# Kernel tuning notes

Hardware: AMD Instinct MI355X
Metric: run time of the kernel (lower is better)

The kernel has to match this reference:

```python
import jax, jax.numpy as jnp
import numpy as np

N, IN_F, OUT_F, R = 8192, 4096, 4096, 16
ALPHA = 32
SCALING = ALPHA / R  # 2.0


def setup_inputs() -> dict:
    key = jax.random.key(0)
    k1, k2, k3, k4, k5 = jax.random.split(key, 5)
    return {
        "x": jax.random.normal(k1, (N, IN_F), dtype=jnp.float32),
        "W": jax.random.normal(k2, (OUT_F, IN_F), dtype=jnp.float32) * 0.02,
        "b": jax.random.normal(k3, (OUT_F,), dtype=jnp.float32) * 0.02,
        "lora_A": jax.random.normal(k4, (R, IN_F), dtype=jnp.float32) * 0.02,
        "lora_B": jax.random.normal(k5, (OUT_F, R), dtype=jnp.float32) * 0.02,
    }


def reference(x, W, b, lora_A, lora_B):
    # Base linear: x [N, in_f] @ W.T [in_f, out_f] + b -> [N, out_f]
    result = jnp.einsum('ni,oi->no', x, W) + b
    # LoRA path: (B @ (A @ x.T)).T * scaling == (x @ A.T) @ B.T * scaling
    lora = jnp.einsum('nr,or->no', jnp.einsum('ni,ri->nr', x, lora_A), lora_B)
    return result + lora * SCALING
```

## Files before the change

### kernel.cpp

```cpp
#include <hip/hip_runtime.h>
#include <hip/hip_bf16.h>
#include <stdint.h>

#define N_ROWS 8192
#define IN_F   4096
#define OUT_F  4096
#define R_LORA 16
#define KP     4160

typedef __bf16 bf16_t;
typedef __attribute__((ext_vector_type(8))) __bf16 bf16x8;
typedef __attribute__((ext_vector_type(4))) __bf16 bf16x4;
typedef __attribute__((ext_vector_type(4))) float  f32x4;
typedef __attribute__((ext_vector_type(16))) float f32x16;

__device__ __forceinline__ void load16_lds(const bf16_t* g, bf16_t* l) {
    auto gp = (const __attribute__((address_space(1))) void*)g;
    auto lp = (__attribute__((address_space(3))) void*)(uint32_t)(uintptr_t)l;
    __builtin_amdgcn_global_load_lds(gp, lp, 16, 0, 0);
}

#define PREPA_BLOCKS 2048

__global__ __launch_bounds__(256) void prep_fused(const float* __restrict__ x,
                                                  const float* __restrict__ W,
                                                  const float* __restrict__ bias,
                                                  const float* __restrict__ lA,
                                                  const float* __restrict__ lB,
                                                  bf16_t* __restrict__ Aw,
                                                  bf16_t* __restrict__ Bw) {
    int b = blockIdx.x;
    int t = threadIdx.x;
    if (b < PREPA_BLOCKS) {
        int row0 = b * 4;
        for (int rr = 0; rr < 4; ++rr) {
            int row = row0 + rr;
            const float4* xr = (const float4*)(x + (size_t)row * IN_F);
            bf16_t* ar = Aw + (size_t)row * KP;
            for (int s = t; s < 512; s += 256) {
                float4 f0 = xr[2 * s];
                float4 f1 = xr[2 * s + 1];
                bf16x8 v;
                v[0] = (bf16_t)f0.x; v[1] = (bf16_t)f0.y;
                v[2] = (bf16_t)f0.z; v[3] = (bf16_t)f0.w;
                v[4] = (bf16_t)f1.x; v[5] = (bf16_t)f1.y;
                v[6] = (bf16_t)f1.z; v[7] = (bf16_t)f1.w;
                *(bf16x8*)(ar + s * 8) = v;
            }
            if (t < 64) ar[IN_F + t] = (t == 0) ? (bf16_t)1.0f : (bf16_t)0.0f;
        }
    } else {
        int o0 = (b - PREPA_BLOCKS) * 4;
        float bl[4][R_LORA];
        for (int oo = 0; oo < 4; ++oo)
            for (int r = 0; r < R_LORA; ++r)
                bl[oo][r] = 2.0f * lB[(o0 + oo) * R_LORA + r];

        for (int j = 0; j < IN_F / (256 * 4); ++j) {
            int i4 = (j * 256 + t) * 4;
            f32x4 acc[4];
            for (int oo = 0; oo < 4; ++oo) {
                float4 w = *(const float4*)(W + (size_t)(o0 + oo) * IN_F + i4);
                acc[oo] = (f32x4){w.x, w.y, w.z, w.w};
            }
            for (int r = 0; r < R_LORA; ++r) {
                float4 a = *(const float4*)(lA + (size_t)r * IN_F + i4);
                for (int oo = 0; oo < 4; ++oo) {
                    acc[oo][0] += bl[oo][r] * a.x;
                    acc[oo][1] += bl[oo][r] * a.y;
                    acc[oo][2] += bl[oo][r] * a.z;
                    acc[oo][3] += bl[oo][r] * a.w;
                }
            }
            for (int oo = 0; oo < 4; ++oo) {
                bf16x4 v;
                v[0] = (bf16_t)acc[oo][0]; v[1] = (bf16_t)acc[oo][1];
                v[2] = (bf16_t)acc[oo][2]; v[3] = (bf16_t)acc[oo][3];
                *(bf16x4*)(Bw + (size_t)(o0 + oo) * KP + i4) = v;
            }
        }
        {
            int oo = t >> 6;
            int c  = IN_F + (t & 63);
            float v = (c == IN_F) ? bias[o0 + oo] : 0.0f;
            Bw[(size_t)(o0 + oo) * KP + c] = (bf16_t)v;
        }
    }
}

#define BM 256
#define BN 256
#define BK 64
#define NT (KP / BK)

__global__ __launch_bounds__(512, 2) void gemm_bt(const bf16_t* __restrict__ A,
                                                  const bf16_t* __restrict__ B,
                                                  float* __restrict__ C) {
    __shared__ __align__(16) bf16_t lds[2][2][BM * BK];

    int bid = blockIdx.x;
    int swz = (bid & 7) * 64 + (bid >> 3);
    int bm  = swz & 31;
    int bn  = swz >> 5;
    int rowBase = bm * BM;
    int colBase = bn * BN;

    const int t    = threadIdx.x;
    const int lane = t & 63;
    const int wave = t >> 6;
    const int l31  = lane & 31;
    const int lhi  = lane >> 5;
    const int l7   = lane & 7;
    const int lsw  = l7 ^ (2 * (l31 >> 3));
    const int wr   = wave >> 2;
    const int wc   = wave & 3;

    int rowOffA[4], colOffB[2];
#pragma unroll
    for (int rf = 0; rf < 4; ++rf) rowOffA[rf] = (wr * 128 + rf * 32 + l31) * BK;
#pragma unroll
    for (int cf = 0; cf < 2; ++cf) colOffB[cf] = (wc * 64 + cf * 32 + l31) * BK;

    uint32_t srcA[4], srcB[4];
#pragma unroll
    for (int s = 0; s < 4; ++s) {
        int c = s * 512 + t;
        int r = c >> 3, p = c & 7;
        int ck = p ^ (r & 7) ^ (2 * ((r >> 3) & 3));
        uint32_t off = (uint32_t)(r * KP + (ck << 3));
        srcA[s] = (uint32_t)(rowBase * KP) + off;
        srcB[s] = (uint32_t)(colBase * KP) + off;
    }

    auto stage = [&](int bsel, int k0) {
#pragma unroll
        for (int s = 0; s < 4; ++s)
            load16_lds(A + srcA[s] + k0, &lds[bsel][0][(s * 512 + t) * 8]);
#pragma unroll
        for (int s = 0; s < 4; ++s)
            load16_lds(B + srcB[s] + k0, &lds[bsel][1][(s * 512 + t) * 8]);
    };

    f32x16 acc[4][2];
#pragma unroll
    for (int rf = 0; rf < 4; ++rf)
#pragma unroll
        for (int cf = 0; cf < 2; ++cf)
#pragma unroll
            for (int r = 0; r < 16; ++r) acc[rf][cf][r] = 0.f;

#define COMPUTE(bsel)                                                          \
    do {                                                                       \
        const bf16_t* Ab = &lds[bsel][0][0];                                   \
        const bf16_t* Bb = &lds[bsel][1][0];                                   \
        _Pragma("unroll")                                                      \
        for (int ks = 0; ks < 4; ++ks) {                                       \
            int pos = ((((ks << 1) | lhi)) ^ lsw) << 3;                        \
            bf16x8 af[4], bf[2];                                               \
            _Pragma("unroll")                                                  \
            for (int rf = 0; rf < 4; ++rf)                                     \
                af[rf] = *(const bf16x8*)&Ab[rowOffA[rf] + pos];               \
            _Pragma("unroll")                                                  \
            for (int cf = 0; cf < 2; ++cf)                                     \
                bf[cf] = *(const bf16x8*)&Bb[colOffB[cf] + pos];               \
            __builtin_amdgcn_s_setprio(1);                                     \
            _Pragma("unroll")                                                  \
            for (int rf = 0; rf < 4; ++rf)                                     \
                _Pragma("unroll")                                              \
                for (int cf = 0; cf < 2; ++cf)                                 \
                    acc[rf][cf] = __builtin_amdgcn_mfma_f32_32x32x16_bf16(     \
                        af[rf], bf[cf], acc[rf][cf], 0, 0, 0);                 \
            __builtin_amdgcn_s_setprio(0);                                     \
        }                                                                      \
    } while (0)

    stage(0, 0);

    for (int kt = 0; kt < NT - 1; ++kt) {
        const int cur = kt & 1;
        const int nb  = cur ^ 1;
        __builtin_amdgcn_s_barrier();
        stage(nb, (kt + 1) * BK);
        asm volatile("s_waitcnt vmcnt(8)" ::: "memory");
        __builtin_amdgcn_s_barrier();
        COMPUTE(cur);
    }
    {
        __builtin_amdgcn_s_barrier();
        asm volatile("s_waitcnt vmcnt(0)" ::: "memory");
        __builtin_amdgcn_s_barrier();
        COMPUTE(0);
    }
#undef COMPUTE

#pragma unroll
    for (int rf = 0; rf < 4; ++rf) {
        int rB = rowBase + wr * 128 + rf * 32 + 4 * lhi;
#pragma unroll
        for (int cf = 0; cf < 2; ++cf) {
            int col = colBase + wc * 64 + cf * 32 + l31;
#pragma unroll
            for (int reg = 0; reg < 16; ++reg) {
                int row = rB + (reg & 3) + 8 * (reg >> 2);
                C[(size_t)row * OUT_F + col] = acc[rf][cf][reg];
            }
        }
    }
}

extern "C" void kernel_launch(void* const* d_in, const int* in_sizes, int n_in,
                              void* d_out, int out_size, void* d_ws, size_t ws_size,
                              hipStream_t stream) {
    const float* x  = (const float*)d_in[0];
    const float* W  = (const float*)d_in[1];
    const float* b  = (const float*)d_in[2];
    const float* lA = (const float*)d_in[3];
    const float* lB = (const float*)d_in[4];
    float* out = (float*)d_out;

    bf16_t* Aw = (bf16_t*)d_ws;
    bf16_t* Bw = Aw + (size_t)N_ROWS * KP;

    prep_fused<<<PREPA_BLOCKS + OUT_F / 4, 256, 0, stream>>>(x, W, b, lA, lB, Aw, Bw);
    gemm_bt<<<(N_ROWS / BM) * (OUT_F / BN), 512, 0, stream>>>(Aw, Bw, out);
}
```

Measured before the change: 542.7 us.

## Flatten prep kernel per-thread chunks and ping-pong GEMM phases with barriers

The prep kernel becomes a flat grid where each thread converts one 8-element chunk of x, or the merged W+LoRA weight, or the bias/padding columns. Per-row loops disappear and more blocks are available to spread the memory traffic. The GEMM main loop splits each K-tile into four phases, each bracketed by workgroup barriers and an lgkmcnt wait, so the waves alternate between LDS reads and MFMA bursts. The extra barriers per tile add synchronisation cost and could serialize waves if the interleaving does not pay off.

```diff
diff --git a/kernel.cpp b/kernel.cpp
--- a/kernel.cpp
+++ b/kernel.cpp
@@ -10,7 +10,6 @@
 
 typedef __bf16 bf16_t;
 typedef __attribute__((ext_vector_type(8))) __bf16 bf16x8;
-typedef __attribute__((ext_vector_type(4))) __bf16 bf16x4;
 typedef __attribute__((ext_vector_type(4))) float  f32x4;
 typedef __attribute__((ext_vector_type(16))) float f32x16;
 
@@ -20,71 +19,71 @@
     __builtin_amdgcn_global_load_lds(gp, lp, 16, 0, 0);
 }
 
-#define PREPA_BLOCKS 2048
-
-__global__ __launch_bounds__(256) void prep_fused(const float* __restrict__ x,
-                                                  const float* __restrict__ W,
-                                                  const float* __restrict__ bias,
-                                                  const float* __restrict__ lA,
-                                                  const float* __restrict__ lB,
-                                                  bf16_t* __restrict__ Aw,
-                                                  bf16_t* __restrict__ Bw) {
-    int b = blockIdx.x;
-    int t = threadIdx.x;
-    if (b < PREPA_BLOCKS) {
-        int row0 = b * 4;
-        for (int rr = 0; rr < 4; ++rr) {
-            int row = row0 + rr;
-            const float4* xr = (const float4*)(x + (size_t)row * IN_F);
-            bf16_t* ar = Aw + (size_t)row * KP;
-            for (int s = t; s < 512; s += 256) {
-                float4 f0 = xr[2 * s];
-                float4 f1 = xr[2 * s + 1];
-                bf16x8 v;
-                v[0] = (bf16_t)f0.x; v[1] = (bf16_t)f0.y;
-                v[2] = (bf16_t)f0.z; v[3] = (bf16_t)f0.w;
-                v[4] = (bf16_t)f1.x; v[5] = (bf16_t)f1.y;
-                v[6] = (bf16_t)f1.z; v[7] = (bf16_t)f1.w;
-                *(bf16x8*)(ar + s * 8) = v;
-            }
-            if (t < 64) ar[IN_F + t] = (t == 0) ? (bf16_t)1.0f : (bf16_t)0.0f;
-        }
+#define CA   (N_ROWS * 512)
+#define CAP  (N_ROWS * 8)
+#define CB   (OUT_F * 512)
+#define CBP  (OUT_F * 8)
+#define PREP_CHUNKS (CA + CAP + CB + CBP)
+#define PREP_BLOCKS (PREP_CHUNKS / 256)
+
+__global__ __launch_bounds__(256) void prep_flat(const float* __restrict__ x,
+                                                 const float* __restrict__ W,
+                                                 const float* __restrict__ bias,
+                                                 const float* __restrict__ lA,
+                                                 const float* __restrict__ lB,
+                                                 bf16_t* __restrict__ Aw,
+                                                 bf16_t* __restrict__ Bw) {
+    int id = blockIdx.x * 256 + threadIdx.x;
+    if (id < CA) {
+        int row = id >> 9, c8 = id & 511;
+        const float4* xp = (const float4*)(x + ((size_t)row << 12) + c8 * 8);
+        float4 f0 = xp[0], f1 = xp[1];
+        bf16x8 v;
+        v[0] = (bf16_t)f0.x; v[1] = (bf16_t)f0.y;
+        v[2] = (bf16_t)f0.z; v[3] = (bf16_t)f0.w;
+        v[4] = (bf16_t)f1.x; v[5] = (bf16_t)f1.y;
+        v[6] = (bf16_t)f1.z; v[7] = (bf16_t)f1.w;
+        *(bf16x8*)(Aw + (size_t)row * KP + c8 * 8) = v;
+    } else if (id < CA + CAP) {
+        int p = id - CA, row = p >> 3, ch = p & 7;
+        bf16x8 v;
+#pragma unroll
+        for (int i = 0; i < 8; ++i) v[i] = (bf16_t)0.0f;
+        if (ch == 0) v[0] = (bf16_t)1.0f;
+        *(bf16x8*)(Aw + (size_t)row * KP + IN_F + ch * 8) = v;
+    } else if (id < CA + CAP + CB) {
+        int p = id - (CA + CAP), o = p >> 9, c8 = p & 511;
+        const float4* lbp = (const float4*)(lB + o * R_LORA);
+        float bl[R_LORA];
+#pragma unroll
+        for (int q = 0; q < 4; ++q) {
+            float4 b4 = lbp[q];
+            bl[q * 4 + 0] = 2.0f * b4.x; bl[q * 4 + 1] = 2.0f * b4.y;
+            bl[q * 4 + 2] = 2.0f * b4.z; bl[q * 4 + 3] = 2.0f * b4.w;
+        }
+        const float4* wp = (const float4*)(W + ((size_t)o << 12) + c8 * 8);
+        float4 w0 = wp[0], w1 = wp[1];
+        float a[8] = {w0.x, w0.y, w0.z, w0.w, w1.x, w1.y, w1.z, w1.w};
+#pragma unroll
+        for (int r = 0; r < R_LORA; ++r) {
+            const float4* ap = (const float4*)(lA + (size_t)r * IN_F + c8 * 8);
+            float4 A0 = ap[0], A1 = ap[1];
+            a[0] += bl[r] * A0.x; a[1] += bl[r] * A0.y;
+            a[2] += bl[r] * A0.z; a[3] += bl[r] * A0.w;
+            a[4] += bl[r] * A1.x; a[5] += bl[r] * A1.y;
+            a[6] += bl[r] * A1.z; a[7] += bl[r] * A1.w;
+        }
+        bf16x8 v;
+#pragma unroll
+        for (int i = 0; i < 8; ++i) v[i] = (bf16_t)a[i];
+        *(bf16x8*)(Bw + (size_t)o * KP + c8 * 8) = v;
     } else {
-        int o0 = (b - PREPA_BLOCKS) * 4;
-        float bl[4][R_LORA];
-        for (int oo = 0; oo < 4; ++oo)
-            for (int r = 0; r < R_LORA; ++r)
-                bl[oo][r] = 2.0f * lB[(o0 + oo) * R_LORA + r];
-
-        for (int j = 0; j < IN_F / (256 * 4); ++j) {
-            int i4 = (j * 256 + t) * 4;
-            f32x4 acc[4];
-            for (int oo = 0; oo < 4; ++oo) {
-                float4 w = *(const float4*)(W + (size_t)(o0 + oo) * IN_F + i4);
-                acc[oo] = (f32x4){w.x, w.y, w.z, w.w};
-            }
-            for (int r = 0; r < R_LORA; ++r) {
-                float4 a = *(const float4*)(lA + (size_t)r * IN_F + i4);
-                for (int oo = 0; oo < 4; ++oo) {
-                    acc[oo][0] += bl[oo][r] * a.x;
-                    acc[oo][1] += bl[oo][r] * a.y;
-                    acc[oo][2] += bl[oo][r] * a.z;
-                    acc[oo][3] += bl[oo][r] * a.w;
-                }
-            }
-            for (int oo = 0; oo < 4; ++oo) {
-                bf16x4 v;
-                v[0] = (bf16_t)acc[oo][0]; v[1] = (bf16_t)acc[oo][1];
-                v[2] = (bf16_t)acc[oo][2]; v[3] = (bf16_t)acc[oo][3];
-                *(bf16x4*)(Bw + (size_t)(o0 + oo) * KP + i4) = v;
-            }
-        }
-        {
-            int oo = t >> 6;
-            int c  = IN_F + (t & 63);
-            float v = (c == IN_F) ? bias[o0 + oo] : 0.0f;
-            Bw[(size_t)(o0 + oo) * KP + c] = (bf16_t)v;
-        }
+        int p = id - (CA + CAP + CB), o = p >> 3, ch = p & 7;
+        bf16x8 v;
+#pragma unroll
+        for (int i = 0; i < 8; ++i) v[i] = (bf16_t)0.0f;
+        if (ch == 0) v[0] = (bf16_t)bias[o];
+        *(bf16x8*)(Bw + (size_t)o * KP + IN_F + ch * 8) = v;
     }
 }
 
@@ -149,49 +148,53 @@
 #pragma unroll
             for (int r = 0; r < 16; ++r) acc[rf][cf][r] = 0.f;
 
-#define COMPUTE(bsel)                                                          \
+#define PHASE(ks)                                                              \
     do {                                                                       \
-        const bf16_t* Ab = &lds[bsel][0][0];                                   \
-        const bf16_t* Bb = &lds[bsel][1][0];                                   \
-        _Pragma("unroll")                                                      \
-        for (int ks = 0; ks < 4; ++ks) {                                       \
-            int pos = ((((ks << 1) | lhi)) ^ lsw) << 3;                        \
-            bf16x8 af[4], bf[2];                                               \
-            _Pragma("unroll")                                                  \
-            for (int rf = 0; rf < 4; ++rf)                                     \
-                af[rf] = *(const bf16x8*)&Ab[rowOffA[rf] + pos];               \
-            _Pragma("unroll")                                                  \
-            for (int cf = 0; cf < 2; ++cf)                                     \
-                bf[cf] = *(const bf16x8*)&Bb[colOffB[cf] + pos];               \
-            __builtin_amdgcn_s_setprio(1);                                     \
-            _Pragma("unroll")                                                  \
-            for (int rf = 0; rf < 4; ++rf)                                     \
-                _Pragma("unroll")                                              \
-                for (int cf = 0; cf < 2; ++cf)                                 \
-                    acc[rf][cf] = __builtin_amdgcn_mfma_f32_32x32x16_bf16(     \
-                        af[rf], bf[cf], acc[rf][cf], 0, 0, 0);                 \
-            __builtin_amdgcn_s_setprio(0);                                     \
-        }                                                                      \
+        const int pos = ((((ks) << 1) | lhi) ^ lsw) << 3;                      \
+        bf16x8 af0 = *(const bf16x8*)&Ab[rowOffA[0] + pos];                    \
+        bf16x8 af1 = *(const bf16x8*)&Ab[rowOffA[1] + pos];                    \
+        bf16x8 af2 = *(const bf16x8*)&Ab[rowOffA[2] + pos];                    \
+        bf16x8 af3 = *(const bf16x8*)&Ab[rowOffA[3] + pos];                    \
+        bf16x8 bf0 = *(const bf16x8*)&Bb[colOffB[0] + pos];                    \
+        bf16x8 bf1 = *(const bf16x8*)&Bb[colOffB[1] + pos];                    \
+        __builtin_amdgcn_s_barrier();                                          \
+        asm volatile("s_waitcnt lgkmcnt(0)" ::: "memory");                     \
+        __builtin_amdgcn_sched_barrier(0);                                     \
+        __builtin_amdgcn_s_setprio(1);                                         \
+        acc[0][0] = __builtin_amdgcn_mfma_f32_32x32x16_bf16(af0, bf0, acc[0][0], 0, 0, 0); \
+        acc[0][1] = __builtin_amdgcn_mfma_f32_32x32x16_bf16(af0, bf1, acc[0][1], 0, 0, 0); \
+        acc[1][0] = __builtin_amdgcn_mfma_f32_32x32x16_bf16(af1, bf0, acc[1][0], 0, 0, 0); \
+        acc[1][1] = __builtin_amdgcn_mfma_f32_32x32x16_bf16(af1, bf1, acc[1][1], 0, 0, 0); \
+        acc[2][0] = __builtin_amdgcn_mfma_f32_32x32x16_bf16(af2, bf0, acc[2][0], 0, 0, 0); \
+        acc[2][1] = __builtin_amdgcn_mfma_f32_32x32x16_bf16(af2, bf1, acc[2][1], 0, 0, 0); \
+        acc[3][0] = __builtin_amdgcn_mfma_f32_32x32x16_bf16(af3, bf0, acc[3][0], 0, 0, 0); \
+        acc[3][1] = __builtin_amdgcn_mfma_f32_32x32x16_bf16(af3, bf1, acc[3][1], 0, 0, 0); \
+        __builtin_amdgcn_s_setprio(0);                                         \
+        __builtin_amdgcn_s_barrier();                                          \
     } while (0)
 
     stage(0, 0);
 
-    for (int kt = 0; kt < NT - 1; ++kt) {
+    for (int kt = 0; kt < NT; ++kt) {
         const int cur = kt & 1;
         const int nb  = cur ^ 1;
+        const bf16_t* Ab = &lds[cur][0][0];
+        const bf16_t* Bb = &lds[cur][1][0];
+
+        if (kt + 1 < NT) {
+            stage(nb, (kt + 1) * BK);
+            asm volatile("s_waitcnt vmcnt(8)" ::: "memory");
+        } else {
+            asm volatile("s_waitcnt vmcnt(0)" ::: "memory");
+        }
         __builtin_amdgcn_s_barrier();
-        stage(nb, (kt + 1) * BK);
-        asm volatile("s_waitcnt vmcnt(8)" ::: "memory");
-        __builtin_amdgcn_s_barrier();
-        COMPUTE(cur);
-    }
-    {
-        __builtin_amdgcn_s_barrier();
-        asm volatile("s_waitcnt vmcnt(0)" ::: "memory");
-        __builtin_amdgcn_s_barrier();
-        COMPUTE(0);
-    }
-#undef COMPUTE
+
+        PHASE(0);
+        PHASE(1);
+        PHASE(2);
+        PHASE(3);
+    }
+#undef PHASE
 
 #pragma unroll
     for (int rf = 0; rf < 4; ++rf) {
@@ -221,6 +224,6 @@
     bf16_t* Aw = (bf16_t*)d_ws;
     bf16_t* Bw = Aw + (size_t)N_ROWS * KP;
 
-    prep_fused<<<PREPA_BLOCKS + OUT_F / 4, 256, 0, stream>>>(x, W, b, lA, lB, Aw, Bw);
+    prep_flat<<<PREP_BLOCKS, 256, 0, stream>>>(x, W, b, lA, lB, Aw, Bw);
     gemm_bt<<<(N_ROWS / BM) * (OUT_F / BN), 512, 0, stream>>>(Aw, Bw, out);
 }
```

New measurement: 606.8 us. 1.12x slower.
